# Performance work log

Measured on AMD Instinct MI355X. Metric: run time of the kernel, lower is better.

## Reference

```python
import jax, jax.numpy as jnp
import numpy as np

B, N, DIM = 2, 1024, 512
HEADS, DIM_HEAD = 8, 64
HIDDEN = HEADS * DIM_HEAD
TIME_DIM = 512
BIAS_DIM = 16
EPS = 1e-5


def setup_inputs() -> dict:
    key = jax.random.key(0)
    ks = jax.random.split(key, 12)
    inp = {
        "x": jax.random.normal(ks[0], (B, N, DIM), jnp.float32),
        "residx": jnp.broadcast_to(jnp.arange(N, dtype=jnp.float32), (B, N)),
        "time": jax.random.normal(ks[1], (B, 1, TIME_DIM), jnp.float32),
        "attn_bias": jax.random.normal(ks[2], (B, BIAS_DIM, N, N), jnp.float32),
        "seq_mask": jnp.ones((B, N), jnp.float32),
        # params
        "gamma": jnp.ones((DIM,), jnp.float32),
        "Wt": jax.random.normal(ks[3], (2 * DIM, TIME_DIM), jnp.float32) * 0.02,
        "bt": jax.random.normal(ks[4], (2 * DIM,), jnp.float32) * 0.02,
        "Wb": jax.random.normal(ks[5], (HEADS, BIAS_DIM), jnp.float32) * 0.1,
        "bb": jax.random.normal(ks[6], (HEADS,), jnp.float32) * 0.1,
        "Wq": jax.random.normal(ks[7], (HIDDEN, DIM), jnp.float32) * (DIM ** -0.5),
        "Wkv": jax.random.normal(ks[8], (2 * HIDDEN, DIM), jnp.float32) * (DIM ** -0.5),
        "Wo": jax.random.normal(ks[9], (DIM, HIDDEN), jnp.float32) * (HIDDEN ** -0.5),
    }
    return inp


def _layer_norm(x, gamma):
    mu = jnp.mean(x, axis=-1, keepdims=True)
    var = jnp.var(x, axis=-1, keepdims=True)
    return (x - mu) * jax.lax.rsqrt(var + EPS) * gamma  # beta buffer is zeros


def reference(x, residx, time, attn_bias, seq_mask, gamma, Wt, bt, Wb, bb, Wq, Wkv, Wo):
    h, d = HEADS, DIM_HEAD
    b, n, _ = x.shape
    xn = _layer_norm(x, gamma)
    # time conditioning: SiLU -> Linear -> chunk into scale/shift
    t = jax.nn.silu(time) @ Wt.T + bt  # [B,1,2*dim]
    scale, shift = jnp.split(t, 2, axis=-1)
    xn = xn * (scale + 1.0) + shift
    xn = xn * seq_mask[..., None]
    # projections
    q = (xn @ Wq.T).reshape(b, n, h, d).transpose(0, 2, 1, 3)  # b h n d
    kv = xn @ Wkv.T
    k_, v_ = jnp.split(kv, 2, axis=-1)
    k = k_.reshape(b, n, h, d).transpose(0, 2, 1, 3)
    v = v_.reshape(b, n, h, d).transpose(0, 2, 1, 3)
    q = q * (d ** -0.5)
    sim = jnp.einsum('bhid,bhjd->bhij', q, k)
    # attn bias projection: b a i j -> linear over a -> b h i j
    bias = jnp.einsum('baij,ha->bhij', attn_bias, Wb) + bb[None, :, None, None]
    sim = sim + bias
    # mask
    attn_mask = seq_mask[:, None, :, None] * seq_mask[:, None, None, :]  # b 1 i j
    sim = sim - (1.0 - attn_mask) * 1e6
    attn = jax.nn.softmax(sim, axis=-1)
    out = jnp.einsum('bhij,bhjd->bhid', attn, v)
    out = out.transpose(0, 2, 1, 3).reshape(b, n, h * d)
    out = out @ Wo.T
    out = out * seq_mask[..., None]
    return out
```

## Files before the change

kernel.cpp:

```cpp
#include <hip/hip_runtime.h>
#include <cstdint>
#include <cstddef>

typedef __bf16 bf16x8 __attribute__((ext_vector_type(8)));
typedef float f32x4 __attribute__((ext_vector_type(4)));
typedef unsigned short u16;
typedef unsigned short u16x8 __attribute__((ext_vector_type(8)));

__device__ __forceinline__ u16 f2b(float f) {
    union { float f; uint32_t u; } v; v.f = f;
    uint32_t r = v.u + 0x7fffu + ((v.u >> 16) & 1u);
    return (u16)(r >> 16);
}
__device__ __forceinline__ float b2f(u16 h) {
    union { uint32_t u; float f; } v; v.u = ((uint32_t)h) << 16; return v.f;
}

__global__ __launch_bounds__(256) void prep_kernel(
    const float* __restrict__ Wq, const float* __restrict__ Wkv, const float* __restrict__ Wo,
    const float* __restrict__ timep, const float* __restrict__ Wt, const float* __restrict__ bt,
    u16* __restrict__ wqkv, u16* __restrict__ wo, float* __restrict__ tbuf)
{
    __shared__ float st[512];
    int bx = blockIdx.x, tid = threadIdx.x;
    if (bx < 1024) {
        int i = bx * 256 + tid;
        float4 v; u16* dp;
        if (i < 65536)      { v = ((const float4*)Wq)[i];            dp = wqkv + (size_t)i * 4; }
        else if (i < 196608){ int k = i - 65536;  v = ((const float4*)Wkv)[k]; dp = wqkv + 262144 + (size_t)k * 4; }
        else                { int k = i - 196608; v = ((const float4*)Wo)[k];  dp = wo + (size_t)k * 4; }
        ushort4 o;
        o.x = f2b(v.x); o.y = f2b(v.y); o.z = f2b(v.z); o.w = f2b(v.w);
        *(ushort4*)dp = o;
    } else {
        int bx2 = bx - 1024;
        int b = bx2 >> 2, ch = bx2 & 3;
        for (int k = tid; k < 512; k += 256) {
            float v = timep[b * 512 + k];
            st[k] = v / (1.f + __expf(-v));
        }
        __syncthreads();
        int o = ch * 256 + tid;
        const float4* wrow = (const float4*)(Wt + (size_t)o * 512);
        float acc = bt[o];
        #pragma unroll 4
        for (int k4 = 0; k4 < 128; k4++) {
            float4 w = wrow[k4];
            acc += st[k4*4+0]*w.x + st[k4*4+1]*w.y + st[k4*4+2]*w.z + st[k4*4+3]*w.w;
        }
        tbuf[b * 1024 + o] = acc;
    }
}

__global__ __launch_bounds__(64) void ln_cond_kernel(
    const float* __restrict__ x, const float* __restrict__ gamma,
    const float* __restrict__ tbuf, const float* __restrict__ seq_mask,
    u16* __restrict__ xn)
{
    int m = blockIdx.x;
    int b = m >> 10;
    int lane = threadIdx.x;
    const float* xr = x + (size_t)m * 512;
    int c0 = lane * 8;
    float4 v0 = *(const float4*)(xr + c0);
    float4 v1 = *(const float4*)(xr + c0 + 4);
    float xv[8] = {v0.x, v0.y, v0.z, v0.w, v1.x, v1.y, v1.z, v1.w};
    float s = 0.f, ss = 0.f;
    #pragma unroll
    for (int e = 0; e < 8; e++) { s += xv[e]; ss += xv[e]*xv[e]; }
    #pragma unroll
    for (int off = 1; off < 64; off <<= 1) {
        s  += __shfl_xor(s, off);
        ss += __shfl_xor(ss, off);
    }
    float mu = s * (1.f/512.f);
    float var = ss * (1.f/512.f) - mu*mu;
    float rs = rsqrtf(var + 1e-5f);
    float mk = seq_mask[m];
    u16x8 ov;
    #pragma unroll
    for (int e = 0; e < 8; e++) {
        int c = c0 + e;
        float sc = tbuf[b*1024 + c] + 1.f;
        float sh = tbuf[b*1024 + 512 + c];
        float val = ((xv[e] - mu) * rs * gamma[c] * sc + sh) * mk;
        ov[e] = f2b(val);
    }
    *(u16x8*)&xn[(size_t)m * 512 + c0] = ov;
}

__global__ __launch_bounds__(256) void qkv_gemm_kernel(
    const u16* __restrict__ xn, const u16* __restrict__ wqkv,
    u16* __restrict__ qb, u16* __restrict__ kb, u16* __restrict__ vT)
{
    __shared__ u16 As[64][40];
    __shared__ u16 Bs[64][40];
    const int tid = threadIdx.x;
    const int lane = tid & 63, wid = tid >> 6;
    const int wr = wid >> 1, wc = wid & 1;
    const int li = lane & 15, g = lane >> 4;
    const int m0 = blockIdx.x * 64, n0 = blockIdx.y * 64;

    f32x4 acc[2][2] = {};
    const int lrow = tid >> 2, lcol = (tid & 3) * 8;
    for (int k0 = 0; k0 < 512; k0 += 32) {
        *(bf16x8*)&As[lrow][lcol] = *(const bf16x8*)&xn[(size_t)(m0+lrow)*512 + k0 + lcol];
        *(bf16x8*)&Bs[lrow][lcol] = *(const bf16x8*)&wqkv[(size_t)(n0+lrow)*512 + k0 + lcol];
        __syncthreads();
        bf16x8 a[2], b[2];
        #pragma unroll
        for (int fi = 0; fi < 2; fi++) a[fi] = *(const bf16x8*)&As[wr*32 + fi*16 + li][g*8];
        #pragma unroll
        for (int fj = 0; fj < 2; fj++) b[fj] = *(const bf16x8*)&Bs[wc*32 + fj*16 + li][g*8];
        #pragma unroll
        for (int fi = 0; fi < 2; fi++)
            #pragma unroll
            for (int fj = 0; fj < 2; fj++)
                acc[fi][fj] = __builtin_amdgcn_mfma_f32_16x16x32_bf16(a[fi], b[fj], acc[fi][fj], 0, 0, 0);
        __syncthreads();
    }
    #pragma unroll
    for (int fi = 0; fi < 2; fi++)
        #pragma unroll
        for (int fj = 0; fj < 2; fj++) {
            int nl = wc*32 + fj*16 + li;
            int o = n0 + nl;
            int m_base = m0 + wr*32 + fi*16 + g*4;
            if (o < 1024) {
                #pragma unroll
                for (int r = 0; r < 4; r++) {
                    int m = m_base + r;
                    int b = m >> 10, n = m & 1023;
                    float v = acc[fi][fj][r];
                    if (o < 512) {
                        qb[((size_t)(b*8 + (o>>6))*1024 + n)*64 + (o&63)] = f2b(v * 0.125f);
                    } else {
                        int oo = o - 512;
                        kb[((size_t)(b*8 + (oo>>6))*1024 + n)*64 + (oo&63)] = f2b(v);
                    }
                }
            } else {
                int oo = o - 1024;
                int b = m_base >> 10, n = m_base & 1023;
                ushort4 ov;
                ov.x = f2b(acc[fi][fj][0]); ov.y = f2b(acc[fi][fj][1]);
                ov.z = f2b(acc[fi][fj][2]); ov.w = f2b(acc[fi][fj][3]);
                *(ushort4*)&vT[((size_t)(b*8 + (oo>>6))*64 + (oo&63))*1024 + n] = ov;
            }
        }
}

__global__ __launch_bounds__(256) void bias_kernel(
    const float* __restrict__ ab, const float* __restrict__ Wb,
    const float* __restrict__ bbv, u16* __restrict__ bias_t)
{
    __shared__ float wbs[128];
    __shared__ float bbs[8];
    int tid = threadIdx.x;
    if (tid < 128) wbs[tid] = Wb[tid];
    if (tid < 8) bbs[tid] = bbv[tid];
    __syncthreads();
    int idx = blockIdx.x * 256 + tid;
    int b = idx >> 18;
    int r = idx & 262143;
    int i = r >> 8;
    int j = (r & 255) * 4;
    f32x4 acc[8];
    #pragma unroll
    for (int h = 0; h < 8; h++) { acc[h][0] = bbs[h]; acc[h][1] = bbs[h]; acc[h][2] = bbs[h]; acc[h][3] = bbs[h]; }
    #pragma unroll
    for (int a = 0; a < 16; a++) {
        const f32x4* src = (const f32x4*)&ab[(((size_t)(b*16 + a)) << 20) + ((size_t)i << 10) + j];
        f32x4 v = __builtin_nontemporal_load(src);
        #pragma unroll
        for (int h = 0; h < 8; h++) {
            float w = wbs[h*16 + a];
            acc[h][0] += w*v[0]; acc[h][1] += w*v[1]; acc[h][2] += w*v[2]; acc[h][3] += w*v[3];
        }
    }
    int it = i >> 6, il = i & 63, jt = j >> 6, jl = j & 63;
    #pragma unroll
    for (int h = 0; h < 8; h++) {
        ushort4 o;
        o.x = f2b(acc[h][0]); o.y = f2b(acc[h][1]); o.z = f2b(acc[h][2]); o.w = f2b(acc[h][3]);
        size_t off = ((((size_t)(b*8 + h)*16 + it)*16 + jt) << 12) + il*64 + jl;
        *(ushort4*)&bias_t[off] = o;
    }
}

__global__ __launch_bounds__(256) void attn_kernel(
    const u16* __restrict__ qb, const u16* __restrict__ kb, const u16* __restrict__ vT,
    const u16* __restrict__ bias_t, const float* __restrict__ seq_mask,
    u16* __restrict__ attn_out)
{
    __shared__ u16 Qs[64][72];
    __shared__ u16 Ks[2][64][72];
    __shared__ u16 Vs[2][64][72];
    __shared__ u16 Bs[2][64][72];
    __shared__ u16 Ps[4][16][72];
    __shared__ float mjs[1024];
    int tid = threadIdx.x;
    int lane = tid & 63, w = tid >> 6;
    int li = lane & 15, g = lane >> 4;
    int it = blockIdx.x, h = blockIdx.y, b = blockIdx.z;
    int i0 = it * 64;
    const u16* qp = qb + ((size_t)(b*8 + h)*1024 + i0) * 64;
    const u16* kp = kb + (size_t)(b*8 + h)*1024*64;
    const u16* vp = vT + (size_t)(b*8 + h)*64*1024;
    const u16* bp = bias_t + ((((size_t)(b*8 + h))*16 + it) << 16);

    *(bf16x8*)&Qs[tid>>2][(tid&3)*16]     = *(const bf16x8*)&qp[tid*16];
    *(bf16x8*)&Qs[tid>>2][(tid&3)*16 + 8] = *(const bf16x8*)&qp[tid*16 + 8];
    ((float4*)mjs)[tid] = ((const float4*)(seq_mask + b*1024))[tid];

    const int krow = tid >> 2, kcol = (tid & 3) * 16;
    const int vrow = tid >> 3, vcol = (tid & 7) * 8;

    bf16x8 kr0, kr1, vr0, vr1, br0, br1;
    #define LOADT(jt_) do { \
        kr0 = *(const bf16x8*)&kp[(size_t)(jt_)*4096 + tid*16]; \
        kr1 = *(const bf16x8*)&kp[(size_t)(jt_)*4096 + tid*16 + 8]; \
        br0 = *(const bf16x8*)&bp[(size_t)(jt_)*4096 + tid*16]; \
        br1 = *(const bf16x8*)&bp[(size_t)(jt_)*4096 + tid*16 + 8]; \
        vr0 = *(const bf16x8*)&vp[(size_t)vrow*1024 + (jt_)*64 + vcol]; \
        vr1 = *(const bf16x8*)&vp[(size_t)(vrow+32)*1024 + (jt_)*64 + vcol]; \
    } while (0)
    #define STORET(buf_) do { \
        *(bf16x8*)&Ks[buf_][krow][kcol]     = kr0; \
        *(bf16x8*)&Ks[buf_][krow][kcol + 8] = kr1; \
        *(bf16x8*)&Bs[buf_][krow][kcol]     = br0; \
        *(bf16x8*)&Bs[buf_][krow][kcol + 8] = br1; \
        *(bf16x8*)&Vs[buf_][vrow][vcol]      = vr0; \
        *(bf16x8*)&Vs[buf_][vrow + 32][vcol] = vr1; \
    } while (0)

    f32x4 oacc[4] = {};
    float m_run[4], l_run[4];
    #pragma unroll
    for (int r = 0; r < 4; r++) { m_run[r] = -3e38f; l_run[r] = 0.f; }
    float mi[4];
    #pragma unroll
    for (int r = 0; r < 4; r++) mi[r] = seq_mask[b*1024 + i0 + w*16 + g*4 + r];

    LOADT(0); STORET(0);
    __syncthreads();

    for (int jt = 0; jt < 16; jt++) {
        int cur = jt & 1;
        if (jt < 15) LOADT(jt + 1);
        f32x4 s[4] = {};
        bf16x8 aq0 = *(const bf16x8*)&Qs[w*16 + li][g*8];
        bf16x8 aq1 = *(const bf16x8*)&Qs[w*16 + li][32 + g*8];
        #pragma unroll
        for (int fj = 0; fj < 4; fj++) {
            bf16x8 bk0 = *(const bf16x8*)&Ks[cur][fj*16 + li][g*8];
            bf16x8 bk1 = *(const bf16x8*)&Ks[cur][fj*16 + li][32 + g*8];
            s[fj] = __builtin_amdgcn_mfma_f32_16x16x32_bf16(aq0, bk0, s[fj], 0, 0, 0);
            s[fj] = __builtin_amdgcn_mfma_f32_16x16x32_bf16(aq1, bk1, s[fj], 0, 0, 0);
        }
        float pmax[4] = {-3e38f, -3e38f, -3e38f, -3e38f};
        #pragma unroll
        for (int fj = 0; fj < 4; fj++) {
            float mj = mjs[jt*64 + fj*16 + li];
            #pragma unroll
            for (int r = 0; r < 4; r++) {
                float sv = s[fj][r] + b2f(Bs[cur][w*16 + g*4 + r][fj*16 + li]);
                sv -= (1.f - mi[r]*mj) * 1e6f;
                s[fj][r] = sv;
                pmax[r] = fmaxf(pmax[r], sv);
            }
        }
        #pragma unroll
        for (int r = 0; r < 4; r++)
            #pragma unroll
            for (int off = 1; off < 16; off <<= 1)
                pmax[r] = fmaxf(pmax[r], __shfl_xor(pmax[r], off));
        float alpha[4], psum[4] = {0.f, 0.f, 0.f, 0.f}, mnew[4];
        #pragma unroll
        for (int r = 0; r < 4; r++) {
            mnew[r] = fmaxf(m_run[r], pmax[r]);
            alpha[r] = __expf(m_run[r] - mnew[r]);
            m_run[r] = mnew[r];
        }
        #pragma unroll
        for (int fj = 0; fj < 4; fj++)
            #pragma unroll
            for (int r = 0; r < 4; r++) {
                float p = __expf(s[fj][r] - mnew[r]);
                s[fj][r] = p;
                psum[r] += p;
            }
        #pragma unroll
        for (int r = 0; r < 4; r++) {
            #pragma unroll
            for (int off = 1; off < 16; off <<= 1) psum[r] += __shfl_xor(psum[r], off);
            l_run[r] = l_run[r]*alpha[r] + psum[r];
        }
        #pragma unroll
        for (int fj = 0; fj < 4; fj++)
            #pragma unroll
            for (int r = 0; r < 4; r++)
                Ps[w][g*4 + r][fj*16 + li] = f2b(s[fj][r]);
        #pragma unroll
        for (int fd = 0; fd < 4; fd++)
            #pragma unroll
            for (int r = 0; r < 4; r++)
                oacc[fd][r] *= alpha[r];
        bf16x8 ap0 = *(const bf16x8*)&Ps[w][li][g*8];
        bf16x8 ap1 = *(const bf16x8*)&Ps[w][li][32 + g*8];
        #pragma unroll
        for (int fd = 0; fd < 4; fd++) {
            bf16x8 bv0 = *(const bf16x8*)&Vs[cur][fd*16 + li][g*8];
            bf16x8 bv1 = *(const bf16x8*)&Vs[cur][fd*16 + li][32 + g*8];
            oacc[fd] = __builtin_amdgcn_mfma_f32_16x16x32_bf16(ap0, bv0, oacc[fd], 0, 0, 0);
            oacc[fd] = __builtin_amdgcn_mfma_f32_16x16x32_bf16(ap1, bv1, oacc[fd], 0, 0, 0);
        }
        if (jt < 15) STORET(cur ^ 1);
        __syncthreads();
    }
    #pragma unroll
    for (int fd = 0; fd < 4; fd++)
        #pragma unroll
        for (int r = 0; r < 4; r++) {
            int i = i0 + w*16 + g*4 + r;
            int col = h*64 + fd*16 + li;
            float val = oacc[fd][r] / l_run[r];
            attn_out[((size_t)(b*1024 + i))*512 + col] = f2b(val);
        }
    #undef LOADT
    #undef STORET
}

__global__ __launch_bounds__(256) void out_gemm_kernel(
    const u16* __restrict__ aout, const u16* __restrict__ wo,
    const float* __restrict__ seq_mask, float* __restrict__ out)
{
    __shared__ u16 As[64][40];
    __shared__ u16 Bs[64][40];
    const int tid = threadIdx.x;
    const int lane = tid & 63, wid = tid >> 6;
    const int wr = wid >> 1, wc = wid & 1;
    const int li = lane & 15, g = lane >> 4;
    const int m0 = blockIdx.x * 64, n0 = blockIdx.y * 64;

    f32x4 acc[2][2] = {};
    const int lrow = tid >> 2, lcol = (tid & 3) * 8;
    for (int k0 = 0; k0 < 512; k0 += 32) {
        *(bf16x8*)&As[lrow][lcol] = *(const bf16x8*)&aout[(size_t)(m0+lrow)*512 + k0 + lcol];
        *(bf16x8*)&Bs[lrow][lcol] = *(const bf16x8*)&wo[(size_t)(n0+lrow)*512 + k0 + lcol];
        __syncthreads();
        bf16x8 a[2], b[2];
        #pragma unroll
        for (int fi = 0; fi < 2; fi++) a[fi] = *(const bf16x8*)&As[wr*32 + fi*16 + li][g*8];
        #pragma unroll
        for (int fj = 0; fj < 2; fj++) b[fj] = *(const bf16x8*)&Bs[wc*32 + fj*16 + li][g*8];
        #pragma unroll
        for (int fi = 0; fi < 2; fi++)
            #pragma unroll
            for (int fj = 0; fj < 2; fj++)
                acc[fi][fj] = __builtin_amdgcn_mfma_f32_16x16x32_bf16(a[fi], b[fj], acc[fi][fj], 0, 0, 0);
        __syncthreads();
    }
    #pragma unroll
    for (int fi = 0; fi < 2; fi++)
        #pragma unroll
        for (int fj = 0; fj < 2; fj++)
            #pragma unroll
            for (int r = 0; r < 4; r++) {
                int m = m0 + wr*32 + fi*16 + g*4 + r;
                int o = n0 + wc*32 + fj*16 + li;
                out[(size_t)m*512 + o] = acc[fi][fj][r] * seq_mask[m];
            }
}

extern "C" void kernel_launch(void* const* d_in, const int* in_sizes, int n_in,
                              void* d_out, int out_size, void* d_ws, size_t ws_size,
                              hipStream_t stream) {
    const float* x         = (const float*)d_in[0];
    const float* timep     = (const float*)d_in[2];
    const float* attn_bias = (const float*)d_in[3];
    const float* seq_mask  = (const float*)d_in[4];
    const float* gamma     = (const float*)d_in[5];
    const float* Wt        = (const float*)d_in[6];
    const float* bt        = (const float*)d_in[7];
    const float* Wb        = (const float*)d_in[8];
    const float* bb        = (const float*)d_in[9];
    const float* Wq        = (const float*)d_in[10];
    const float* Wkv       = (const float*)d_in[11];
    const float* Wo        = (const float*)d_in[12];
    float* out = (float*)d_out;

    char* ws = (char*)d_ws;
    size_t off = 0;
    auto alloc = [&](size_t bytes) { char* p = ws + off; off += (bytes + 255) & ~(size_t)255; return p; };
    float* tbuf  = (float*)alloc(2 * 1024 * 4);
    u16* xn      = (u16*)alloc((size_t)2048 * 512 * 2);
    u16* wqkv    = (u16*)alloc((size_t)1536 * 512 * 2);
    u16* wo      = (u16*)alloc((size_t)512 * 512 * 2);
    u16* qb      = (u16*)alloc((size_t)2 * 8 * 1024 * 64 * 2);
    u16* kb      = (u16*)alloc((size_t)2 * 8 * 1024 * 64 * 2);
    u16* vT      = (u16*)alloc((size_t)2 * 8 * 64 * 1024 * 2);
    u16* bias_t  = (u16*)alloc((size_t)2 * 8 * 1024 * 1024 * 2);
    u16* aout    = (u16*)alloc((size_t)2048 * 512 * 2);
    (void)ws_size;

    prep_kernel<<<1032, 256, 0, stream>>>(Wq, Wkv, Wo, timep, Wt, bt, wqkv, wo, tbuf);
    ln_cond_kernel<<<2048, 64, 0, stream>>>(x, gamma, tbuf, seq_mask, xn);
    qkv_gemm_kernel<<<dim3(32, 24), 256, 0, stream>>>(xn, wqkv, qb, kb, vT);
    bias_kernel<<<2048, 256, 0, stream>>>(attn_bias, Wb, bb, bias_t);
    attn_kernel<<<dim3(16, 8, 2), 256, 0, stream>>>(qb, kb, vT, bias_t, seq_mask, aout);
    out_gemm_kernel<<<dim3(32, 8), 256, 0, stream>>>(aout, wo, seq_mask, out);
}
```

Measured before the change: 104.6 us.

## Enlarge QKV GEMM tiles, retile bias layout, split-KV attention with register-fed MFMA

The QKV GEMM moves from 64x64 to 128x128 block tiles, so each wave computes a 4x4 grid of MFMA fragments and reuses more of each staged tile. The bias kernel now has each thread handle a 4x4 patch and writes bias in a fragment-ordered layout that the attention kernel loads straight into registers. The attention kernel drops shared-memory staging of K, V and bias and loads fragments directly from global memory. It splits the key range across two waves per query tile and merges the partial softmax results through shared memory at the end. This adds more concurrent blocks and removes the per-tile barriers, at the cost of uncoalesced global loads with no double buffering and a final merge step.

```diff
diff --git a/kernel.cpp b/kernel.cpp
--- a/kernel.cpp
+++ b/kernel.cpp
@@ -93,45 +93,46 @@
     const u16* __restrict__ xn, const u16* __restrict__ wqkv,
     u16* __restrict__ qb, u16* __restrict__ kb, u16* __restrict__ vT)
 {
-    __shared__ u16 As[64][40];
-    __shared__ u16 Bs[64][40];
+    __shared__ u16 As[128][40];
+    __shared__ u16 Bs[128][40];
     const int tid = threadIdx.x;
     const int lane = tid & 63, wid = tid >> 6;
     const int wr = wid >> 1, wc = wid & 1;
     const int li = lane & 15, g = lane >> 4;
-    const int m0 = blockIdx.x * 64, n0 = blockIdx.y * 64;
-
-    f32x4 acc[2][2] = {};
-    const int lrow = tid >> 2, lcol = (tid & 3) * 8;
+    const int m0 = blockIdx.x * 128, n0 = blockIdx.y * 128;
+
+    f32x4 acc[4][4] = {};
+    const int srow = tid >> 2, scol = (tid & 3) * 8;
     for (int k0 = 0; k0 < 512; k0 += 32) {
-        *(bf16x8*)&As[lrow][lcol] = *(const bf16x8*)&xn[(size_t)(m0+lrow)*512 + k0 + lcol];
-        *(bf16x8*)&Bs[lrow][lcol] = *(const bf16x8*)&wqkv[(size_t)(n0+lrow)*512 + k0 + lcol];
+        *(bf16x8*)&As[srow][scol]      = *(const bf16x8*)&xn[(size_t)(m0+srow)*512 + k0 + scol];
+        *(bf16x8*)&As[srow+64][scol]   = *(const bf16x8*)&xn[(size_t)(m0+srow+64)*512 + k0 + scol];
+        *(bf16x8*)&Bs[srow][scol]      = *(const bf16x8*)&wqkv[(size_t)(n0+srow)*512 + k0 + scol];
+        *(bf16x8*)&Bs[srow+64][scol]   = *(const bf16x8*)&wqkv[(size_t)(n0+srow+64)*512 + k0 + scol];
         __syncthreads();
-        bf16x8 a[2], b[2];
-        #pragma unroll
-        for (int fi = 0; fi < 2; fi++) a[fi] = *(const bf16x8*)&As[wr*32 + fi*16 + li][g*8];
-        #pragma unroll
-        for (int fj = 0; fj < 2; fj++) b[fj] = *(const bf16x8*)&Bs[wc*32 + fj*16 + li][g*8];
-        #pragma unroll
-        for (int fi = 0; fi < 2; fi++)
-            #pragma unroll
-            for (int fj = 0; fj < 2; fj++)
-                acc[fi][fj] = __builtin_amdgcn_mfma_f32_16x16x32_bf16(a[fi], b[fj], acc[fi][fj], 0, 0, 0);
+        bf16x8 a[4], bf[4];
+        #pragma unroll
+        for (int mi = 0; mi < 4; mi++) a[mi]  = *(const bf16x8*)&As[wr*64 + mi*16 + li][g*8];
+        #pragma unroll
+        for (int nj = 0; nj < 4; nj++) bf[nj] = *(const bf16x8*)&Bs[wc*64 + nj*16 + li][g*8];
+        #pragma unroll
+        for (int mi = 0; mi < 4; mi++)
+            #pragma unroll
+            for (int nj = 0; nj < 4; nj++)
+                acc[mi][nj] = __builtin_amdgcn_mfma_f32_16x16x32_bf16(a[mi], bf[nj], acc[mi][nj], 0, 0, 0);
         __syncthreads();
     }
     #pragma unroll
-    for (int fi = 0; fi < 2; fi++)
-        #pragma unroll
-        for (int fj = 0; fj < 2; fj++) {
-            int nl = wc*32 + fj*16 + li;
-            int o = n0 + nl;
-            int m_base = m0 + wr*32 + fi*16 + g*4;
+    for (int mi = 0; mi < 4; mi++)
+        #pragma unroll
+        for (int nj = 0; nj < 4; nj++) {
+            int o = n0 + wc*64 + nj*16 + li;
+            int m_base = m0 + wr*64 + mi*16 + g*4;
             if (o < 1024) {
                 #pragma unroll
                 for (int r = 0; r < 4; r++) {
                     int m = m_base + r;
                     int b = m >> 10, n = m & 1023;
-                    float v = acc[fi][fj][r];
+                    float v = acc[mi][nj][r];
                     if (o < 512) {
                         qb[((size_t)(b*8 + (o>>6))*1024 + n)*64 + (o&63)] = f2b(v * 0.125f);
                     } else {
@@ -143,8 +144,8 @@
                 int oo = o - 1024;
                 int b = m_base >> 10, n = m_base & 1023;
                 ushort4 ov;
-                ov.x = f2b(acc[fi][fj][0]); ov.y = f2b(acc[fi][fj][1]);
-                ov.z = f2b(acc[fi][fj][2]); ov.w = f2b(acc[fi][fj][3]);
+                ov.x = f2b(acc[mi][nj][0]); ov.y = f2b(acc[mi][nj][1]);
+                ov.z = f2b(acc[mi][nj][2]); ov.w = f2b(acc[mi][nj][3]);
                 *(ushort4*)&vT[((size_t)(b*8 + (oo>>6))*64 + (oo&63))*1024 + n] = ov;
             }
         }
@@ -160,31 +161,46 @@
     if (tid < 128) wbs[tid] = Wb[tid];
     if (tid < 8) bbs[tid] = bbv[tid];
     __syncthreads();
-    int idx = blockIdx.x * 256 + tid;
-    int b = idx >> 18;
-    int r = idx & 262143;
-    int i = r >> 8;
-    int j = (r & 255) * 4;
-    f32x4 acc[8];
-    #pragma unroll
-    for (int h = 0; h < 8; h++) { acc[h][0] = bbs[h]; acc[h][1] = bbs[h]; acc[h][2] = bbs[h]; acc[h][3] = bbs[h]; }
-    #pragma unroll
+    int t = blockIdx.x * 256 + tid;
+    int b = t >> 16;
+    int rem = t & 65535;
+    int iq = rem >> 8, jq = rem & 255;
+    int i = iq * 4, j = jq * 4;
+    f32x4 acc[8][4];
+    #pragma unroll
+    for (int h = 0; h < 8; h++)
+        #pragma unroll
+        for (int r = 0; r < 4; r++) {
+            float bv = bbs[h];
+            acc[h][r][0] = bv; acc[h][r][1] = bv; acc[h][r][2] = bv; acc[h][r][3] = bv;
+        }
     for (int a = 0; a < 16; a++) {
-        const f32x4* src = (const f32x4*)&ab[(((size_t)(b*16 + a)) << 20) + ((size_t)i << 10) + j];
-        f32x4 v = __builtin_nontemporal_load(src);
+        f32x4 v[4];
+        #pragma unroll
+        for (int r = 0; r < 4; r++) {
+            const f32x4* src = (const f32x4*)&ab[(((size_t)(b*16 + a)) << 20) + ((size_t)(i + r) << 10) + j];
+            v[r] = __builtin_nontemporal_load(src);
+        }
         #pragma unroll
         for (int h = 0; h < 8; h++) {
             float w = wbs[h*16 + a];
-            acc[h][0] += w*v[0]; acc[h][1] += w*v[1]; acc[h][2] += w*v[2]; acc[h][3] += w*v[3];
-        }
-    }
-    int it = i >> 6, il = i & 63, jt = j >> 6, jl = j & 63;
+            #pragma unroll
+            for (int r = 0; r < 4; r++) acc[h][r] += w * v[r];
+        }
+    }
+    int it32 = iq >> 3, jt = jq >> 4;
+    int isub = (iq >> 2) & 1, g = iq & 3;
+    int li0 = (jq & 3) * 4, fj = (jq >> 2) & 3;
     #pragma unroll
     for (int h = 0; h < 8; h++) {
-        ushort4 o;
-        o.x = f2b(acc[h][0]); o.y = f2b(acc[h][1]); o.z = f2b(acc[h][2]); o.w = f2b(acc[h][3]);
-        size_t off = ((((size_t)(b*8 + h)*16 + it)*16 + jt) << 12) + il*64 + jl;
-        *(ushort4*)&bias_t[off] = o;
+        size_t base = ((((size_t)(b*8 + h))*32 + it32)*16 + jt)*2048 + fj*4;
+        #pragma unroll
+        for (int c = 0; c < 4; c++) {
+            ushort4 o;
+            o.x = f2b(acc[h][0][c]); o.y = f2b(acc[h][1][c]);
+            o.z = f2b(acc[h][2][c]); o.w = f2b(acc[h][3][c]);
+            *(ushort4*)&bias_t[base + (size_t)(isub*64 + g*16 + li0 + c)*16] = o;
+        }
     }
 }
 
@@ -193,78 +209,67 @@
     const u16* __restrict__ bias_t, const float* __restrict__ seq_mask,
     u16* __restrict__ attn_out)
 {
-    __shared__ u16 Qs[64][72];
-    __shared__ u16 Ks[2][64][72];
-    __shared__ u16 Vs[2][64][72];
-    __shared__ u16 Bs[2][64][72];
     __shared__ u16 Ps[4][16][72];
     __shared__ float mjs[1024];
+    __shared__ float Om[2][16][72];
+    __shared__ float ml[2][16][2];
     int tid = threadIdx.x;
-    int lane = tid & 63, w = tid >> 6;
+    int lane = tid & 63, wid = tid >> 6;
+    int qt = wid >> 1, jh = wid & 1;
     int li = lane & 15, g = lane >> 4;
-    int it = blockIdx.x, h = blockIdx.y, b = blockIdx.z;
-    int i0 = it * 64;
-    const u16* qp = qb + ((size_t)(b*8 + h)*1024 + i0) * 64;
-    const u16* kp = kb + (size_t)(b*8 + h)*1024*64;
-    const u16* vp = vT + (size_t)(b*8 + h)*64*1024;
-    const u16* bp = bias_t + ((((size_t)(b*8 + h))*16 + it) << 16);
-
-    *(bf16x8*)&Qs[tid>>2][(tid&3)*16]     = *(const bf16x8*)&qp[tid*16];
-    *(bf16x8*)&Qs[tid>>2][(tid&3)*16 + 8] = *(const bf16x8*)&qp[tid*16 + 8];
+    int bx = blockIdx.x, h = blockIdx.y, b = blockIdx.z;
+    int bh = b*8 + h;
+    int i0 = bx*32 + qt*16;
+    const u16* qp = qb + ((size_t)bh*1024 + i0)*64;
+    const u16* kp = kb + (size_t)bh*65536;
+    const u16* vp = vT + (size_t)bh*65536;
+    const u16* bp = bias_t + (((size_t)bh*32 + bx)*16)*2048 + (qt*64 + lane)*16;
+
     ((float4*)mjs)[tid] = ((const float4*)(seq_mask + b*1024))[tid];
 
-    const int krow = tid >> 2, kcol = (tid & 3) * 16;
-    const int vrow = tid >> 3, vcol = (tid & 7) * 8;
-
-    bf16x8 kr0, kr1, vr0, vr1, br0, br1;
-    #define LOADT(jt_) do { \
-        kr0 = *(const bf16x8*)&kp[(size_t)(jt_)*4096 + tid*16]; \
-        kr1 = *(const bf16x8*)&kp[(size_t)(jt_)*4096 + tid*16 + 8]; \
-        br0 = *(const bf16x8*)&bp[(size_t)(jt_)*4096 + tid*16]; \
-        br1 = *(const bf16x8*)&bp[(size_t)(jt_)*4096 + tid*16 + 8]; \
-        vr0 = *(const bf16x8*)&vp[(size_t)vrow*1024 + (jt_)*64 + vcol]; \
-        vr1 = *(const bf16x8*)&vp[(size_t)(vrow+32)*1024 + (jt_)*64 + vcol]; \
-    } while (0)
-    #define STORET(buf_) do { \
-        *(bf16x8*)&Ks[buf_][krow][kcol]     = kr0; \
-        *(bf16x8*)&Ks[buf_][krow][kcol + 8] = kr1; \
-        *(bf16x8*)&Bs[buf_][krow][kcol]     = br0; \
-        *(bf16x8*)&Bs[buf_][krow][kcol + 8] = br1; \
-        *(bf16x8*)&Vs[buf_][vrow][vcol]      = vr0; \
-        *(bf16x8*)&Vs[buf_][vrow + 32][vcol] = vr1; \
-    } while (0)
+    bf16x8 aq0 = *(const bf16x8*)&qp[li*64 + g*8];
+    bf16x8 aq1 = *(const bf16x8*)&qp[li*64 + 32 + g*8];
 
     f32x4 oacc[4] = {};
-    float m_run[4], l_run[4];
-    #pragma unroll
-    for (int r = 0; r < 4; r++) { m_run[r] = -3e38f; l_run[r] = 0.f; }
-    float mi[4];
-    #pragma unroll
-    for (int r = 0; r < 4; r++) mi[r] = seq_mask[b*1024 + i0 + w*16 + g*4 + r];
-
-    LOADT(0); STORET(0);
+    float m_run[4], l_run[4], mi[4];
+    #pragma unroll
+    for (int r = 0; r < 4; r++) {
+        m_run[r] = -3e38f; l_run[r] = 0.f;
+        mi[r] = seq_mask[b*1024 + i0 + g*4 + r];
+    }
     __syncthreads();
 
-    for (int jt = 0; jt < 16; jt++) {
-        int cur = jt & 1;
-        if (jt < 15) LOADT(jt + 1);
+    for (int jtt = 0; jtt < 8; jtt++) {
+        int jt = jh*8 + jtt;
+        bf16x8 bk0[4], bk1[4], bv0[4], bv1[4];
+        #pragma unroll
+        for (int fj = 0; fj < 4; fj++) {
+            bk0[fj] = *(const bf16x8*)&kp[(size_t)(jt*64 + fj*16 + li)*64 + g*8];
+            bk1[fj] = *(const bf16x8*)&kp[(size_t)(jt*64 + fj*16 + li)*64 + 32 + g*8];
+        }
+        bf16x8 bfA = *(const bf16x8*)&bp[(size_t)jt*2048];
+        bf16x8 bfB = *(const bf16x8*)&bp[(size_t)jt*2048 + 8];
+        #pragma unroll
+        for (int fd = 0; fd < 4; fd++) {
+            bv0[fd] = *(const bf16x8*)&vp[(size_t)(fd*16 + li)*1024 + jt*64 + g*8];
+            bv1[fd] = *(const bf16x8*)&vp[(size_t)(fd*16 + li)*1024 + jt*64 + 32 + g*8];
+        }
         f32x4 s[4] = {};
-        bf16x8 aq0 = *(const bf16x8*)&Qs[w*16 + li][g*8];
-        bf16x8 aq1 = *(const bf16x8*)&Qs[w*16 + li][32 + g*8];
+        __builtin_amdgcn_s_setprio(1);
         #pragma unroll
         for (int fj = 0; fj < 4; fj++) {
-            bf16x8 bk0 = *(const bf16x8*)&Ks[cur][fj*16 + li][g*8];
-            bf16x8 bk1 = *(const bf16x8*)&Ks[cur][fj*16 + li][32 + g*8];
-            s[fj] = __builtin_amdgcn_mfma_f32_16x16x32_bf16(aq0, bk0, s[fj], 0, 0, 0);
-            s[fj] = __builtin_amdgcn_mfma_f32_16x16x32_bf16(aq1, bk1, s[fj], 0, 0, 0);
-        }
+            s[fj] = __builtin_amdgcn_mfma_f32_16x16x32_bf16(aq0, bk0[fj], s[fj], 0, 0, 0);
+            s[fj] = __builtin_amdgcn_mfma_f32_16x16x32_bf16(aq1, bk1[fj], s[fj], 0, 0, 0);
+        }
+        __builtin_amdgcn_s_setprio(0);
         float pmax[4] = {-3e38f, -3e38f, -3e38f, -3e38f};
         #pragma unroll
         for (int fj = 0; fj < 4; fj++) {
             float mj = mjs[jt*64 + fj*16 + li];
             #pragma unroll
             for (int r = 0; r < 4; r++) {
-                float sv = s[fj][r] + b2f(Bs[cur][w*16 + g*4 + r][fj*16 + li]);
+                float bvl = (fj < 2) ? b2f(((u16x8)bfA)[(fj&1)*4 + r]) : b2f(((u16x8)bfB)[(fj&1)*4 + r]);
+                float sv = s[fj][r] + bvl;
                 sv -= (1.f - mi[r]*mj) * 1e6f;
                 s[fj][r] = sv;
                 pmax[r] = fmaxf(pmax[r], sv);
@@ -300,35 +305,53 @@
         for (int fj = 0; fj < 4; fj++)
             #pragma unroll
             for (int r = 0; r < 4; r++)
-                Ps[w][g*4 + r][fj*16 + li] = f2b(s[fj][r]);
+                Ps[wid][g*4 + r][fj*16 + li] = f2b(s[fj][r]);
         #pragma unroll
         for (int fd = 0; fd < 4; fd++)
             #pragma unroll
             for (int r = 0; r < 4; r++)
                 oacc[fd][r] *= alpha[r];
-        bf16x8 ap0 = *(const bf16x8*)&Ps[w][li][g*8];
-        bf16x8 ap1 = *(const bf16x8*)&Ps[w][li][32 + g*8];
+        bf16x8 ap0 = *(const bf16x8*)&Ps[wid][li][g*8];
+        bf16x8 ap1 = *(const bf16x8*)&Ps[wid][li][32 + g*8];
+        __builtin_amdgcn_s_setprio(1);
         #pragma unroll
         for (int fd = 0; fd < 4; fd++) {
-            bf16x8 bv0 = *(const bf16x8*)&Vs[cur][fd*16 + li][g*8];
-            bf16x8 bv1 = *(const bf16x8*)&Vs[cur][fd*16 + li][32 + g*8];
-            oacc[fd] = __builtin_amdgcn_mfma_f32_16x16x32_bf16(ap0, bv0, oacc[fd], 0, 0, 0);
-            oacc[fd] = __builtin_amdgcn_mfma_f32_16x16x32_bf16(ap1, bv1, oacc[fd], 0, 0, 0);
-        }
-        if (jt < 15) STORET(cur ^ 1);
-        __syncthreads();
-    }
-    #pragma unroll
-    for (int fd = 0; fd < 4; fd++)
+            oacc[fd] = __builtin_amdgcn_mfma_f32_16x16x32_bf16(ap0, bv0[fd], oacc[fd], 0, 0, 0);
+            oacc[fd] = __builtin_amdgcn_mfma_f32_16x16x32_bf16(ap1, bv1[fd], oacc[fd], 0, 0, 0);
+        }
+        __builtin_amdgcn_s_setprio(0);
+    }
+    if (jh == 1) {
+        #pragma unroll
+        for (int fd = 0; fd < 4; fd++)
+            #pragma unroll
+            for (int r = 0; r < 4; r++)
+                Om[qt][g*4 + r][fd*16 + li] = oacc[fd][r];
+        if (li == 0) {
+            #pragma unroll
+            for (int r = 0; r < 4; r++) {
+                ml[qt][g*4 + r][0] = m_run[r];
+                ml[qt][g*4 + r][1] = l_run[r];
+            }
+        }
+    }
+    __syncthreads();
+    if (jh == 0) {
         #pragma unroll
         for (int r = 0; r < 4; r++) {
-            int i = i0 + w*16 + g*4 + r;
-            int col = h*64 + fd*16 + li;
-            float val = oacc[fd][r] / l_run[r];
-            attn_out[((size_t)(b*1024 + i))*512 + col] = f2b(val);
-        }
-    #undef LOADT
-    #undef STORET
+            float m2 = ml[qt][g*4 + r][0], l2 = ml[qt][g*4 + r][1];
+            float mm = fmaxf(m_run[r], m2);
+            float e1 = __expf(m_run[r] - mm), e2 = __expf(m2 - mm);
+            float linv = 1.f / (l_run[r]*e1 + l2*e2);
+            int i = i0 + g*4 + r;
+            #pragma unroll
+            for (int fd = 0; fd < 4; fd++) {
+                float o2 = Om[qt][g*4 + r][fd*16 + li];
+                float val = (oacc[fd][r]*e1 + o2*e2) * linv;
+                attn_out[((size_t)(b*1024 + i))*512 + h*64 + fd*16 + li] = f2b(val);
+            }
+        }
+    }
 }
 
 __global__ __launch_bounds__(256) void out_gemm_kernel(
@@ -349,16 +372,16 @@
         *(bf16x8*)&As[lrow][lcol] = *(const bf16x8*)&aout[(size_t)(m0+lrow)*512 + k0 + lcol];
         *(bf16x8*)&Bs[lrow][lcol] = *(const bf16x8*)&wo[(size_t)(n0+lrow)*512 + k0 + lcol];
         __syncthreads();
-        bf16x8 a[2], b[2];
-        #pragma unroll
-        for (int fi = 0; fi < 2; fi++) a[fi] = *(const bf16x8*)&As[wr*32 + fi*16 + li][g*8];
-        #pragma unroll
-        for (int fj = 0; fj < 2; fj++) b[fj] = *(const bf16x8*)&Bs[wc*32 + fj*16 + li][g*8];
+        bf16x8 a[2], bf[2];
+        #pragma unroll
+        for (int fi = 0; fi < 2; fi++) a[fi]  = *(const bf16x8*)&As[wr*32 + fi*16 + li][g*8];
+        #pragma unroll
+        for (int fj = 0; fj < 2; fj++) bf[fj] = *(const bf16x8*)&Bs[wc*32 + fj*16 + li][g*8];
         #pragma unroll
         for (int fi = 0; fi < 2; fi++)
             #pragma unroll
             for (int fj = 0; fj < 2; fj++)
-                acc[fi][fj] = __builtin_amdgcn_mfma_f32_16x16x32_bf16(a[fi], b[fj], acc[fi][fj], 0, 0, 0);
+                acc[fi][fj] = __builtin_amdgcn_mfma_f32_16x16x32_bf16(a[fi], bf[fj], acc[fi][fj], 0, 0, 0);
         __syncthreads();
     }
     #pragma unroll
@@ -406,8 +429,8 @@
 
     prep_kernel<<<1032, 256, 0, stream>>>(Wq, Wkv, Wo, timep, Wt, bt, wqkv, wo, tbuf);
     ln_cond_kernel<<<2048, 64, 0, stream>>>(x, gamma, tbuf, seq_mask, xn);
-    qkv_gemm_kernel<<<dim3(32, 24), 256, 0, stream>>>(xn, wqkv, qb, kb, vT);
-    bias_kernel<<<2048, 256, 0, stream>>>(attn_bias, Wb, bb, bias_t);
-    attn_kernel<<<dim3(16, 8, 2), 256, 0, stream>>>(qb, kb, vT, bias_t, seq_mask, aout);
+    qkv_gemm_kernel<<<dim3(16, 12), 256, 0, stream>>>(xn, wqkv, qb, kb, vT);
+    bias_kernel<<<512, 256, 0, stream>>>(attn_bias, Wb, bb, bias_t);
+    attn_kernel<<<dim3(32, 8, 2), 256, 0, stream>>>(qb, kb, vT, bias_t, seq_mask, aout);
     out_gemm_kernel<<<dim3(32, 8), 256, 0, stream>>>(aout, wo, seq_mask, out);
 }
```

Result: slower. 115.0 us (+9.9%).
